# Optimization experiments

Hardware: AMD Instinct MI355X
Metric: run time of the kernel (lower is better)

Reference implementation:

```python
import jax, jax.numpy as jnp
from jax import lax
import numpy as np

I, H, O, B, T = 8, 64, 8, 256, 2048


def setup_inputs() -> dict:
    key = jax.random.key(0)
    ks = jax.random.split(key, 12)
    s_ih = 1.0 / np.sqrt(H)
    u = lambda k, shape: jax.random.uniform(k, shape, jnp.float32, -s_ih, s_ih)
    return {
        "x": jax.random.normal(ks[0], (B, T, I), jnp.float32),
        "W_ih0": u(ks[1], (H, I)),
        "W_hh0": u(ks[2], (H, H)),
        "b_ih0": u(ks[3], (H,)),
        "b_hh0": u(ks[4], (H,)),
        "W_ih1": u(ks[5], (H, H)),
        "W_hh1": u(ks[6], (H, H)),
        "b_ih1": u(ks[7], (H,)),
        "b_hh1": u(ks[8], (H,)),
        "W_fc": u(ks[9], (O, H)),
        "b_fc": u(ks[10], (O,)),
    }


def reference(x, W_ih0, W_hh0, b_ih0, b_hh0, W_ih1, W_hh1, b_ih1, b_hh1, W_fc, b_fc):
    Bx = x.shape[0]
    xt = jnp.swapaxes(x, 0, 1)  # [T, B, I]
    h_init = (jnp.zeros((Bx, H), x.dtype), jnp.zeros((Bx, H), x.dtype))

    def step(carry, x_t):
        h0, h1 = carry
        h0n = jnp.tanh(x_t @ W_ih0.T + b_ih0 + h0 @ W_hh0.T + b_hh0)
        h1n = jnp.tanh(h0n @ W_ih1.T + b_ih1 + h1 @ W_hh1.T + b_hh1)
        return (h0n, h1n), h1n

    (h0f, h1f), outs = lax.scan(step, h_init, xt)  # outs: [T, B, H]
    out = jnp.swapaxes(outs, 0, 1).reshape(-1, H) @ W_fc.T + b_fc  # [B*T, O]
    hidden = jnp.stack([h0f, h1f])  # [2, B, H]
    return out, hidden
```

## Files before the change

### kernel.cpp

```cpp
#include <hip/hip_runtime.h>

#define NI 8
#define NH 64
#define NO 8
#define NB 256
#define NT 2048

typedef float v2f __attribute__((ext_vector_type(2)));

__device__ __forceinline__ v2f fma2(v2f a, v2f b, v2f c) {
    return __builtin_elementwise_fma(a, b, c);
}

__device__ __forceinline__ float tanh_fast(float s) {
    float e = __expf(2.0f * s);
    return fmaf(-2.0f, __builtin_amdgcn_rcpf(e + 1.0f), 1.0f);
}

__device__ __forceinline__ float rlane(float v, int k) {
    return __int_as_float(__builtin_amdgcn_readlane(__float_as_int(v), k));
}

__attribute__((amdgpu_waves_per_eu(1, 1)))
__global__ void __launch_bounds__(256) rnn_quad(
    const float* __restrict__ x,
    const float* __restrict__ W_ih0, const float* __restrict__ W_hh0,
    const float* __restrict__ b_ih0, const float* __restrict__ b_hh0,
    const float* __restrict__ W_ih1, const float* __restrict__ W_hh1,
    const float* __restrict__ b_ih1, const float* __restrict__ b_hh1,
    const float* __restrict__ W_fc,  const float* __restrict__ b_fc,
    float* __restrict__ out)
{
    const int b    = blockIdx.x;
    const int tid  = threadIdx.x;
    const int wid  = tid >> 6;
    const int lane = tid & 63;
    const int o    = lane & 7;
    const int kg   = lane >> 3;

    __shared__ float h0r[16][NH];
    __shared__ float pir[16][NH];
    __shared__ float h1r[16][NH];
    __shared__ float ur[32][NH];
    __shared__ int   fa, fb, fc, fd, fu;

    if (tid == 0) { fa = -1; fb = -1; fc = -1; fd = -1; fu = -1; }
    __syncthreads();

    volatile int* vfa = &fa;
    volatile int* vfb = &fb;
    volatile int* vfc = &fc;
    volatile int* vfd = &fd;
    volatile int* vfu = &fu;

    const float*  xb   = x   + (size_t)b * NT * NI;
    float*        outb = out + (size_t)b * NT * NO;
    const size_t  hid  = (size_t)NB * NT * NO;

    if (wid == 0) {
        float w[NH];
        #pragma unroll
        for (int k = 0; k < NH; ++k) w[k] = W_hh0[lane * NH + k];
        float h0n = 0.0f;

        for (int t = 0; t < NT; ++t) {
            if ((t & 7) == 0) {
                const int needU = (t + 7 < NT) ? t + 7 : NT - 1;
                while (*vfu < needU) {}
                while (*vfb < t - 9) {}
                asm volatile("" ::: "memory");
            }
            const float uv = ur[t & 31][lane];

            float c0 = 0.f, c1 = 0.f, c2 = 0.f, c3 = 0.f;
            #pragma unroll
            for (int k = 0; k < NH; k += 8) {
                const float s0 = rlane(h0n, k + 0), s1 = rlane(h0n, k + 1);
                const float s2 = rlane(h0n, k + 2), s3 = rlane(h0n, k + 3);
                const float s4 = rlane(h0n, k + 4), s5 = rlane(h0n, k + 5);
                const float s6 = rlane(h0n, k + 6), s7 = rlane(h0n, k + 7);
                c0 = fmaf(s0, w[k + 0], c0); c1 = fmaf(s1, w[k + 1], c1);
                c2 = fmaf(s2, w[k + 2], c2); c3 = fmaf(s3, w[k + 3], c3);
                c0 = fmaf(s4, w[k + 4], c0); c1 = fmaf(s5, w[k + 5], c1);
                c2 = fmaf(s6, w[k + 6], c2); c3 = fmaf(s7, w[k + 7], c3);
            }
            h0n = tanh_fast(((c0 + c1) + (c2 + c3)) + uv);

            h0r[t & 15][lane] = h0n;
            asm volatile("s_waitcnt lgkmcnt(0)" ::: "memory");
            *vfa = t;
        }
        out[hid + (size_t)b * NH + lane] = h0n;
    } else if (wid == 1) {
        v2f w2[NH / 2];
        #pragma unroll
        for (int k = 0; k < NH / 2; ++k)
            w2[k] = v2f{W_ih1[lane * NH + 2 * k], W_ih1[lane * NH + 2 * k + 1]};

        for (int t = 0; t < NT; ++t) {
            while (*vfa < t) {}
            if ((t & 7) == 0) {
                while (*vfc < t - 9) {}
            }
            asm volatile("" ::: "memory");

            const float4* hp = (const float4*)(&h0r[t & 15][0]);
            v2f a0 = {0.f, 0.f}, a1 = {0.f, 0.f}, a2 = {0.f, 0.f}, a3 = {0.f, 0.f};
            #pragma unroll
            for (int k = 0; k < 16; ++k) {
                const float4 g = hp[k];
                const v2f lo = {g.x, g.y}, hi = {g.z, g.w};
                if (k & 1) { a2 = fma2(lo, w2[2 * k], a2); a3 = fma2(hi, w2[2 * k + 1], a3); }
                else       { a0 = fma2(lo, w2[2 * k], a0); a1 = fma2(hi, w2[2 * k + 1], a1); }
            }
            const v2f sv = (a0 + a1) + (a2 + a3);
            pir[t & 15][lane] = sv.x + sv.y;
            asm volatile("s_waitcnt lgkmcnt(0)" ::: "memory");
            *vfb = t;
        }
    } else if (wid == 2) {
        float w[NH];
        #pragma unroll
        for (int k = 0; k < NH; ++k) w[k] = W_hh1[lane * NH + k];
        const float bias1 = b_ih1[lane] + b_hh1[lane];
        float h1n = 0.0f;

        for (int t = 0; t < NT; ++t) {
            while (*vfb < t) {}
            if ((t & 7) == 0) {
                while (*vfd < t - 9) {}
            }
            asm volatile("" ::: "memory");
            const float pv = pir[t & 15][lane];

            float c0 = bias1, c1 = 0.f, c2 = 0.f, c3 = 0.f;
            #pragma unroll
            for (int k = 0; k < NH; k += 8) {
                const float s0 = rlane(h1n, k + 0), s1 = rlane(h1n, k + 1);
                const float s2 = rlane(h1n, k + 2), s3 = rlane(h1n, k + 3);
                const float s4 = rlane(h1n, k + 4), s5 = rlane(h1n, k + 5);
                const float s6 = rlane(h1n, k + 6), s7 = rlane(h1n, k + 7);
                c0 = fmaf(s0, w[k + 0], c0); c1 = fmaf(s1, w[k + 1], c1);
                c2 = fmaf(s2, w[k + 2], c2); c3 = fmaf(s3, w[k + 3], c3);
                c0 = fmaf(s4, w[k + 4], c0); c1 = fmaf(s5, w[k + 5], c1);
                c2 = fmaf(s6, w[k + 6], c2); c3 = fmaf(s7, w[k + 7], c3);
            }
            h1n = tanh_fast(((c0 + c1) + (c2 + c3)) + pv);

            h1r[t & 15][lane] = h1n;
            asm volatile("s_waitcnt lgkmcnt(0)" ::: "memory");
            *vfc = t;
        }
        out[hid + (size_t)NB * NH + (size_t)b * NH + lane] = h1n;
    } else {
        float wih0r[NI];
        #pragma unroll
        for (int i = 0; i < NI; ++i) wih0r[i] = W_ih0[lane * NI + i];
        const float bias0 = b_ih0[lane] + b_hh0[lane];
        float wfcr[8];
        #pragma unroll
        for (int m = 0; m < 8; ++m) wfcr[m] = W_fc[o * NH + kg * 8 + m];
        const float bfc = b_fc[o];

        for (int s = 0; s < 16; ++s) {
            const float4 xa = *(const float4*)(xb + (size_t)s * NI);
            const float4 xc = *(const float4*)(xb + (size_t)s * NI + 4);
            float u = bias0;
            u = fmaf(xa.x, wih0r[0], u); u = fmaf(xa.y, wih0r[1], u);
            u = fmaf(xa.z, wih0r[2], u); u = fmaf(xa.w, wih0r[3], u);
            u = fmaf(xc.x, wih0r[4], u); u = fmaf(xc.y, wih0r[5], u);
            u = fmaf(xc.z, wih0r[6], u); u = fmaf(xc.w, wih0r[7], u);
            ur[s][lane] = u;
        }
        asm volatile("s_waitcnt lgkmcnt(0)" ::: "memory");
        *vfu = 15;

        float4 px0 = {0,0,0,0}, px1 = {0,0,0,0};
        if (16 < NT) {
            px0 = *(const float4*)(xb + (size_t)16 * NI);
            px1 = *(const float4*)(xb + (size_t)16 * NI + 4);
        }

        for (int t = 0; t < NT; ++t) {
            const int tp = t + 16;
            if (tp < NT) {
                float u = bias0;
                u = fmaf(px0.x, wih0r[0], u); u = fmaf(px0.y, wih0r[1], u);
                u = fmaf(px0.z, wih0r[2], u); u = fmaf(px0.w, wih0r[3], u);
                u = fmaf(px1.x, wih0r[4], u); u = fmaf(px1.y, wih0r[5], u);
                u = fmaf(px1.z, wih0r[6], u); u = fmaf(px1.w, wih0r[7], u);
                ur[tp & 31][lane] = u;
                if (tp + 1 < NT) {
                    px0 = *(const float4*)(xb + (size_t)(tp + 1) * NI);
                    px1 = *(const float4*)(xb + (size_t)(tp + 1) * NI + 4);
                }
            }
            if ((t & 3) == 3) {
                asm volatile("s_waitcnt lgkmcnt(0)" ::: "memory");
                *vfu = (tp < NT) ? tp : NT - 1;
            }

            while (*vfc < t) {}
            asm volatile("" ::: "memory");
            const float4 u0 = *(const float4*)(&h1r[t & 15][kg * 8]);
            const float4 u1 = *(const float4*)(&h1r[t & 15][kg * 8 + 4]);
            float p = u0.x * wfcr[0] + u0.y * wfcr[1] + u0.z * wfcr[2] + u0.w * wfcr[3]
                    + u1.x * wfcr[4] + u1.y * wfcr[5] + u1.z * wfcr[6] + u1.w * wfcr[7];
            p += __shfl_xor(p, 8);
            p += __shfl_xor(p, 16);
            p += __shfl_xor(p, 32);
            if (lane < NO) outb[(size_t)t * NO + o] = p + bfc;

            if ((t & 3) == 3) {
                asm volatile("s_waitcnt lgkmcnt(0)" ::: "memory");
                *vfd = t;
            }
        }
    }
}

extern "C" void kernel_launch(void* const* d_in, const int* in_sizes, int n_in,
                              void* d_out, int out_size, void* d_ws, size_t ws_size,
                              hipStream_t stream) {
    const float* x     = (const float*)d_in[0];
    const float* W_ih0 = (const float*)d_in[1];
    const float* W_hh0 = (const float*)d_in[2];
    const float* b_ih0 = (const float*)d_in[3];
    const float* b_hh0 = (const float*)d_in[4];
    const float* W_ih1 = (const float*)d_in[5];
    const float* W_hh1 = (const float*)d_in[6];
    const float* b_ih1 = (const float*)d_in[7];
    const float* b_hh1 = (const float*)d_in[8];
    const float* W_fc  = (const float*)d_in[9];
    const float* b_fc  = (const float*)d_in[10];

    rnn_quad<<<dim3(NB), dim3(256), 0, stream>>>(
        x, W_ih0, W_hh0, b_ih0, b_hh0,
        W_ih1, W_hh1, b_ih1, b_hh1, W_fc, b_fc,
        (float*)d_out);
}
```

Before: 814.7 us.

## Restructure four-wave RNN pipeline into three waves with fused projections via LDS broadcast

Merges the W_ih1 projection into the layer-0 recurrence wave and the FC output into the layer-1 recurrence wave, cutting the block to three waves and one fewer handoff stage. The hidden-state broadcast now writes h to LDS and reads it back as float4 packed FMAs instead of 64 readlanes. The input-projection wave is throttled by layer-0 progress. Per-step work on the critical recurrence waves doubles (two dot products each), but the change removes inter-wave flag handoffs and readlane latency from each step.

```diff
diff --git a/kernel.cpp b/kernel.cpp
--- a/kernel.cpp
+++ b/kernel.cpp
@@ -17,12 +17,8 @@
     return fmaf(-2.0f, __builtin_amdgcn_rcpf(e + 1.0f), 1.0f);
 }
 
-__device__ __forceinline__ float rlane(float v, int k) {
-    return __int_as_float(__builtin_amdgcn_readlane(__float_as_int(v), k));
-}
-
 __attribute__((amdgpu_waves_per_eu(1, 1)))
-__global__ void __launch_bounds__(256) rnn_quad(
+__global__ void __launch_bounds__(192) rnn_tri3(
     const float* __restrict__ x,
     const float* __restrict__ W_ih0, const float* __restrict__ W_hh0,
     const float* __restrict__ b_ih0, const float* __restrict__ b_hh0,
@@ -35,132 +31,161 @@
     const int tid  = threadIdx.x;
     const int wid  = tid >> 6;
     const int lane = tid & 63;
-    const int o    = lane & 7;
-    const int kg   = lane >> 3;
-
-    __shared__ float h0r[16][NH];
+
+    __shared__ float ur[32][NH];
     __shared__ float pir[16][NH];
-    __shared__ float h1r[16][NH];
-    __shared__ float ur[32][NH];
-    __shared__ int   fa, fb, fc, fd, fu;
-
-    if (tid == 0) { fa = -1; fb = -1; fc = -1; fd = -1; fu = -1; }
+    __shared__ float h0s[NH];
+    __shared__ float h1s[NH];
+    __shared__ int   fa, fc2, fu;
+
+    if (tid == 0) { fa = -1; fc2 = -1; fu = -1; }
     __syncthreads();
 
-    volatile int* vfa = &fa;
-    volatile int* vfb = &fb;
-    volatile int* vfc = &fc;
-    volatile int* vfd = &fd;
-    volatile int* vfu = &fu;
+    volatile int* vfa  = &fa;
+    volatile int* vfc2 = &fc2;
+    volatile int* vfu  = &fu;
 
     const float*  xb   = x   + (size_t)b * NT * NI;
     float*        outb = out + (size_t)b * NT * NO;
     const size_t  hid  = (size_t)NB * NT * NO;
 
     if (wid == 0) {
-        float w[NH];
+        v2f wh[NH / 2], wi[NH / 2];
         #pragma unroll
-        for (int k = 0; k < NH; ++k) w[k] = W_hh0[lane * NH + k];
+        for (int k = 0; k < NH / 2; ++k) {
+            wh[k] = v2f{W_hh0[lane * NH + 2 * k], W_hh0[lane * NH + 2 * k + 1]};
+            wi[k] = v2f{W_ih1[lane * NH + 2 * k], W_ih1[lane * NH + 2 * k + 1]};
+        }
         float h0n = 0.0f;
 
         for (int t = 0; t < NT; ++t) {
             if ((t & 7) == 0) {
                 const int needU = (t + 7 < NT) ? t + 7 : NT - 1;
                 while (*vfu < needU) {}
-                while (*vfb < t - 9) {}
+                while (*vfc2 < t - 11) {}
                 asm volatile("" ::: "memory");
             }
             const float uv = ur[t & 31][lane];
 
-            float c0 = 0.f, c1 = 0.f, c2 = 0.f, c3 = 0.f;
-            #pragma unroll
-            for (int k = 0; k < NH; k += 8) {
-                const float s0 = rlane(h0n, k + 0), s1 = rlane(h0n, k + 1);
-                const float s2 = rlane(h0n, k + 2), s3 = rlane(h0n, k + 3);
-                const float s4 = rlane(h0n, k + 4), s5 = rlane(h0n, k + 5);
-                const float s6 = rlane(h0n, k + 6), s7 = rlane(h0n, k + 7);
-                c0 = fmaf(s0, w[k + 0], c0); c1 = fmaf(s1, w[k + 1], c1);
-                c2 = fmaf(s2, w[k + 2], c2); c3 = fmaf(s3, w[k + 3], c3);
-                c0 = fmaf(s4, w[k + 4], c0); c1 = fmaf(s5, w[k + 5], c1);
-                c2 = fmaf(s6, w[k + 6], c2); c3 = fmaf(s7, w[k + 7], c3);
-            }
-            h0n = tanh_fast(((c0 + c1) + (c2 + c3)) + uv);
-
-            h0r[t & 15][lane] = h0n;
-            asm volatile("s_waitcnt lgkmcnt(0)" ::: "memory");
-            *vfa = t;
-        }
+            h0s[lane] = h0n;
+            const float4* hp = (const float4*)h0s;
+            v2f aW0 = {0,0}, aW1 = {0,0}, aW2 = {0,0}, aW3 = {0,0};
+            v2f aI0 = {0,0}, aI1 = {0,0}, aI2 = {0,0}, aI3 = {0,0};
+            #pragma unroll
+            for (int k = 0; k < 16; ++k) {
+                const float4 g = hp[k];
+                const v2f lo = {g.x, g.y}, hi = {g.z, g.w};
+                if (k & 1) {
+                    aW2 = fma2(lo, wh[2 * k], aW2); aW3 = fma2(hi, wh[2 * k + 1], aW3);
+                    aI2 = fma2(lo, wi[2 * k], aI2); aI3 = fma2(hi, wi[2 * k + 1], aI3);
+                } else {
+                    aW0 = fma2(lo, wh[2 * k], aW0); aW1 = fma2(hi, wh[2 * k + 1], aW1);
+                    aI0 = fma2(lo, wi[2 * k], aI0); aI1 = fma2(hi, wi[2 * k + 1], aI1);
+                }
+            }
+            const v2f sW = (aW0 + aW1) + (aW2 + aW3);
+            const v2f sI = (aI0 + aI1) + (aI2 + aI3);
+            const float dW = sW.x + sW.y;
+            const float dI = sI.x + sI.y;
+
+            if (t > 0) pir[(t - 1) & 15][lane] = dI;
+            if (t & 1) {
+                asm volatile("s_waitcnt lgkmcnt(0)" ::: "memory");
+                *vfa = t - 1;
+            }
+            h0n = tanh_fast(dW + uv);
+        }
+
+        while (*vfc2 < NT - 17) {}
+        asm volatile("" ::: "memory");
+        h0s[lane] = h0n;
+        {
+            const float4* hp = (const float4*)h0s;
+            v2f aI0 = {0,0}, aI1 = {0,0}, aI2 = {0,0}, aI3 = {0,0};
+            #pragma unroll
+            for (int k = 0; k < 16; ++k) {
+                const float4 g = hp[k];
+                const v2f lo = {g.x, g.y}, hi = {g.z, g.w};
+                if (k & 1) { aI2 = fma2(lo, wi[2 * k], aI2); aI3 = fma2(hi, wi[2 * k + 1], aI3); }
+                else       { aI0 = fma2(lo, wi[2 * k], aI0); aI1 = fma2(hi, wi[2 * k + 1], aI1); }
+            }
+            const v2f sI = (aI0 + aI1) + (aI2 + aI3);
+            pir[(NT - 1) & 15][lane] = sI.x + sI.y;
+        }
+        asm volatile("s_waitcnt lgkmcnt(0)" ::: "memory");
+        *vfa = NT - 1;
         out[hid + (size_t)b * NH + lane] = h0n;
     } else if (wid == 1) {
-        v2f w2[NH / 2];
+        v2f wh1[NH / 2], wf[NH / 2];
+        const int o = lane & 7;
         #pragma unroll
-        for (int k = 0; k < NH / 2; ++k)
-            w2[k] = v2f{W_ih1[lane * NH + 2 * k], W_ih1[lane * NH + 2 * k + 1]};
+        for (int k = 0; k < NH / 2; ++k) {
+            wh1[k] = v2f{W_hh1[lane * NH + 2 * k], W_hh1[lane * NH + 2 * k + 1]};
+            wf[k]  = v2f{W_fc[o * NH + 2 * k],     W_fc[o * NH + 2 * k + 1]};
+        }
+        const float bias1 = b_ih1[lane] + b_hh1[lane];
+        const float bfc   = b_fc[o];
+        float h1n = 0.0f;
 
         for (int t = 0; t < NT; ++t) {
-            while (*vfa < t) {}
-            if ((t & 7) == 0) {
-                while (*vfc < t - 9) {}
-            }
-            asm volatile("" ::: "memory");
-
-            const float4* hp = (const float4*)(&h0r[t & 15][0]);
-            v2f a0 = {0.f, 0.f}, a1 = {0.f, 0.f}, a2 = {0.f, 0.f}, a3 = {0.f, 0.f};
-            #pragma unroll
-            for (int k = 0; k < 16; ++k) {
-                const float4 g = hp[k];
-                const v2f lo = {g.x, g.y}, hi = {g.z, g.w};
-                if (k & 1) { a2 = fma2(lo, w2[2 * k], a2); a3 = fma2(hi, w2[2 * k + 1], a3); }
-                else       { a0 = fma2(lo, w2[2 * k], a0); a1 = fma2(hi, w2[2 * k + 1], a1); }
-            }
-            const v2f sv = (a0 + a1) + (a2 + a3);
-            pir[t & 15][lane] = sv.x + sv.y;
-            asm volatile("s_waitcnt lgkmcnt(0)" ::: "memory");
-            *vfb = t;
-        }
+            if ((t & 3) == 0) {
+                const int need = (t + 3 < NT) ? t + 3 : NT - 1;
+                while (*vfa < need) {}
+                asm volatile("" ::: "memory");
+            }
+            const float pv = pir[t & 15][lane];
+
+            h1s[lane] = h1n;
+            const float4* hp = (const float4*)h1s;
+            v2f aW0 = {0,0}, aW1 = {0,0}, aW2 = {0,0}, aW3 = {0,0};
+            v2f aF0 = {0,0}, aF1 = {0,0}, aF2 = {0,0}, aF3 = {0,0};
+            #pragma unroll
+            for (int k = 0; k < 16; ++k) {
+                const float4 g = hp[k];
+                const v2f lo = {g.x, g.y}, hi = {g.z, g.w};
+                if (k & 1) {
+                    aW2 = fma2(lo, wh1[2 * k], aW2); aW3 = fma2(hi, wh1[2 * k + 1], aW3);
+                    aF2 = fma2(lo, wf[2 * k],  aF2); aF3 = fma2(hi, wf[2 * k + 1],  aF3);
+                } else {
+                    aW0 = fma2(lo, wh1[2 * k], aW0); aW1 = fma2(hi, wh1[2 * k + 1], aW1);
+                    aF0 = fma2(lo, wf[2 * k],  aF0); aF1 = fma2(hi, wf[2 * k + 1],  aF1);
+                }
+            }
+            const v2f sW = (aW0 + aW1) + (aW2 + aW3);
+            const v2f sF = (aF0 + aF1) + (aF2 + aF3);
+            const float dW = sW.x + sW.y;
+            const float dF = sF.x + sF.y;
+
+            if (t > 0 && lane < NO)
+                outb[(size_t)(t - 1) * NO + o] = dF + bfc;
+
+            h1n = tanh_fast(dW + pv + bias1);
+            if ((t & 3) == 3) {
+                asm volatile("s_waitcnt lgkmcnt(0)" ::: "memory");
+                *vfc2 = t;
+            }
+        }
+
+        h1s[lane] = h1n;
+        {
+            const float4* hp = (const float4*)h1s;
+            v2f aF0 = {0,0}, aF1 = {0,0}, aF2 = {0,0}, aF3 = {0,0};
+            #pragma unroll
+            for (int k = 0; k < 16; ++k) {
+                const float4 g = hp[k];
+                const v2f lo = {g.x, g.y}, hi = {g.z, g.w};
+                if (k & 1) { aF2 = fma2(lo, wf[2 * k], aF2); aF3 = fma2(hi, wf[2 * k + 1], aF3); }
+                else       { aF0 = fma2(lo, wf[2 * k], aF0); aF1 = fma2(hi, wf[2 * k + 1], aF1); }
+            }
+            const v2f sF = (aF0 + aF1) + (aF2 + aF3);
+            if (lane < NO) outb[(size_t)(NT - 1) * NO + o] = sF.x + sF.y + bfc;
+        }
+        out[hid + (size_t)NB * NH + (size_t)b * NH + lane] = h1n;
     } else if (wid == 2) {
-        float w[NH];
-        #pragma unroll
-        for (int k = 0; k < NH; ++k) w[k] = W_hh1[lane * NH + k];
-        const float bias1 = b_ih1[lane] + b_hh1[lane];
-        float h1n = 0.0f;
-
-        for (int t = 0; t < NT; ++t) {
-            while (*vfb < t) {}
-            if ((t & 7) == 0) {
-                while (*vfd < t - 9) {}
-            }
-            asm volatile("" ::: "memory");
-            const float pv = pir[t & 15][lane];
-
-            float c0 = bias1, c1 = 0.f, c2 = 0.f, c3 = 0.f;
-            #pragma unroll
-            for (int k = 0; k < NH; k += 8) {
-                const float s0 = rlane(h1n, k + 0), s1 = rlane(h1n, k + 1);
-                const float s2 = rlane(h1n, k + 2), s3 = rlane(h1n, k + 3);
-                const float s4 = rlane(h1n, k + 4), s5 = rlane(h1n, k + 5);
-                const float s6 = rlane(h1n, k + 6), s7 = rlane(h1n, k + 7);
-                c0 = fmaf(s0, w[k + 0], c0); c1 = fmaf(s1, w[k + 1], c1);
-                c2 = fmaf(s2, w[k + 2], c2); c3 = fmaf(s3, w[k + 3], c3);
-                c0 = fmaf(s4, w[k + 4], c0); c1 = fmaf(s5, w[k + 5], c1);
-                c2 = fmaf(s6, w[k + 6], c2); c3 = fmaf(s7, w[k + 7], c3);
-            }
-            h1n = tanh_fast(((c0 + c1) + (c2 + c3)) + pv);
-
-            h1r[t & 15][lane] = h1n;
-            asm volatile("s_waitcnt lgkmcnt(0)" ::: "memory");
-            *vfc = t;
-        }
-        out[hid + (size_t)NB * NH + (size_t)b * NH + lane] = h1n;
-    } else {
         float wih0r[NI];
         #pragma unroll
         for (int i = 0; i < NI; ++i) wih0r[i] = W_ih0[lane * NI + i];
         const float bias0 = b_ih0[lane] + b_hh0[lane];
-        float wfcr[8];
-        #pragma unroll
-        for (int m = 0; m < 8; ++m) wfcr[m] = W_fc[o * NH + kg * 8 + m];
-        const float bfc = b_fc[o];
 
         for (int s = 0; s < 16; ++s) {
             const float4 xa = *(const float4*)(xb + (size_t)s * NI);
@@ -182,38 +207,26 @@
         }
 
         for (int t = 0; t < NT; ++t) {
-            const int tp = t + 16;
-            if (tp < NT) {
+            if ((t & 7) == 0) {
+                while (*vfa < t - 8) {}
+                asm volatile("" ::: "memory");
+            }
+            const int s = t + 16;
+            if (s < NT) {
                 float u = bias0;
                 u = fmaf(px0.x, wih0r[0], u); u = fmaf(px0.y, wih0r[1], u);
                 u = fmaf(px0.z, wih0r[2], u); u = fmaf(px0.w, wih0r[3], u);
                 u = fmaf(px1.x, wih0r[4], u); u = fmaf(px1.y, wih0r[5], u);
                 u = fmaf(px1.z, wih0r[6], u); u = fmaf(px1.w, wih0r[7], u);
-                ur[tp & 31][lane] = u;
-                if (tp + 1 < NT) {
-                    px0 = *(const float4*)(xb + (size_t)(tp + 1) * NI);
-                    px1 = *(const float4*)(xb + (size_t)(tp + 1) * NI + 4);
+                ur[s & 31][lane] = u;
+                if (s + 1 < NT) {
+                    px0 = *(const float4*)(xb + (size_t)(s + 1) * NI);
+                    px1 = *(const float4*)(xb + (size_t)(s + 1) * NI + 4);
                 }
             }
             if ((t & 3) == 3) {
                 asm volatile("s_waitcnt lgkmcnt(0)" ::: "memory");
-                *vfu = (tp < NT) ? tp : NT - 1;
-            }
-
-            while (*vfc < t) {}
-            asm volatile("" ::: "memory");
-            const float4 u0 = *(const float4*)(&h1r[t & 15][kg * 8]);
-            const float4 u1 = *(const float4*)(&h1r[t & 15][kg * 8 + 4]);
-            float p = u0.x * wfcr[0] + u0.y * wfcr[1] + u0.z * wfcr[2] + u0.w * wfcr[3]
-                    + u1.x * wfcr[4] + u1.y * wfcr[5] + u1.z * wfcr[6] + u1.w * wfcr[7];
-            p += __shfl_xor(p, 8);
-            p += __shfl_xor(p, 16);
-            p += __shfl_xor(p, 32);
-            if (lane < NO) outb[(size_t)t * NO + o] = p + bfc;
-
-            if ((t & 3) == 3) {
-                asm volatile("s_waitcnt lgkmcnt(0)" ::: "memory");
-                *vfd = t;
+                *vfu = (s < NT) ? s : NT - 1;
             }
         }
     }
@@ -234,7 +247,7 @@
     const float* W_fc  = (const float*)d_in[9];
     const float* b_fc  = (const float*)d_in[10];
 
-    rnn_quad<<<dim3(NB), dim3(256), 0, stream>>>(
+    rnn_tri3<<<dim3(NB), dim3(192), 0, stream>>>(
         x, W_ih0, W_hh0, b_ih0, b_hh0,
         W_ih1, W_hh1, b_ih1, b_hh1, W_fc, b_fc,
         (float*)d_out);
```

Result: faster. 722.2 us (-11.4%).
